# Kernel optimization log

Measured on AMD Instinct MI355X. Metric: run time of the kernel, lower is better.

Reference implementation:

```python
import jax, jax.numpy as jnp
import numpy as np


def _warp_nn(img, flow):
    """Nearest-neighbor warp of one sample.
    img:  [C, D, H, W] channels to deform
    flow: [3, D, H, W] voxel displacements for dims (D, H, W)
    out(p) = img(round(p + flow(p))), indices clamped to the volume.
    """
    D, H, W = img.shape[1:]
    gd = jnp.arange(D, dtype=flow.dtype)[:, None, None]
    gh = jnp.arange(H, dtype=flow.dtype)[None, :, None]
    gw = jnp.arange(W, dtype=flow.dtype)[None, None, :]
    id_ = jnp.clip(jnp.round(gd + flow[0]), 0, D - 1).astype(jnp.int32)
    ih = jnp.clip(jnp.round(gh + flow[1]), 0, H - 1).astype(jnp.int32)
    iw = jnp.clip(jnp.round(gw + flow[2]), 0, W - 1).astype(jnp.int32)
    return img[:, id_, ih, iw]  # gather, [C, D, H, W]


def reference(x, num_steps):
    # scaling: v = x / 2**num_steps
    B, C = x.shape[0], x.shape[1]
    spatial = x.shape[2:]
    v = x / (2.0 ** num_steps)
    # squaring: v <- v + warp(v, v), applied per 3-channel flow group
    warp = jax.vmap(jax.vmap(_warp_nn))  # over batch, then over groups
    for _ in range(num_steps):
        groups = v.reshape(B, C // 3, 3, *spatial)
        vdef = warp(groups, groups).reshape(v.shape)
        v = v + vdef
    return v


def setup_inputs() -> dict:
    key = jax.random.key(0)
    # displacement field in voxel units; scaled so post-scaling steps still move voxels
    x = jax.random.normal(key, (2, 3, 128, 160, 160), dtype=jnp.float32) * 8.0
    return {"x": x, "num_steps": 6}
```

## Files before the change

### kernel.cpp

```cpp
#include <hip/hip_runtime.h>

#define BB 2
#define DD 128
#define HH 160
#define WW 160
constexpr int S   = DD * HH * WW;
constexpr int PL  = HH * WW;
constexpr int VPB = 512;
constexpr int BPP = PL / VPB;
constexpr int NBLK = BB * DD * BPP;
constexpr int PER_XCD = NBLK / 8;

__device__ __forceinline__ int warp_index(int d, int h, int w,
                                          float f0, float f1, float f2) {
    int id = (int)fminf(fmaxf(rintf((float)d + f0), 0.0f), (float)(DD - 1));
    int ih = (int)fminf(fmaxf(rintf((float)h + f1), 0.0f), (float)(HH - 1));
    int iw = (int)fminf(fmaxf(rintf((float)w + f2), 0.0f), (float)(WW - 1));
    return (id * HH + ih) * WW + iw;
}

template <bool IN_SOA, bool OUT_SOA>
__global__ __launch_bounds__(256) void step_k(const float* __restrict__ vin,
                                              float* __restrict__ vout,
                                              float scale) {
    int bid = blockIdx.x;
    int nb  = (bid >> 3) + (bid & 7) * PER_XCD;
    int b   = nb / (DD * BPP);
    int r   = nb - b * (DD * BPP);
    int d   = r / BPP;
    int ip0 = (r - d * BPP) * VPB + threadIdx.x;
    int ip1 = ip0 + 256;

    int w0 = ip0 % WW, h0 = ip0 / WW;
    int w1 = ip1 % WW, h1 = ip1 / WW;
    int p0 = d * PL + ip0;
    int p1 = d * PL + ip1;

    float a0, a1, a2, c0, c1, c2;
    if constexpr (IN_SOA) {
        int s0 = b * 3 * S + p0, s1 = b * 3 * S + p1;
        a0 = vin[s0] * scale; a1 = vin[s0 + S] * scale; a2 = vin[s0 + 2 * S] * scale;
        c0 = vin[s1] * scale; c1 = vin[s1 + S] * scale; c2 = vin[s1 + 2 * S] * scale;
    } else {
        int i0 = (b * S + p0) * 3, i1 = (b * S + p1) * 3;
        a0 = vin[i0] * scale; a1 = vin[i0 + 1] * scale; a2 = vin[i0 + 2] * scale;
        c0 = vin[i1] * scale; c1 = vin[i1 + 1] * scale; c2 = vin[i1 + 2] * scale;
    }

    int q0 = warp_index(d, h0, w0, a0, a1, a2);
    int q1 = warp_index(d, h1, w1, c0, c1, c2);

    float g0, g1, g2, e0, e1, e2;
    if constexpr (IN_SOA) {
        int s0 = b * 3 * S + q0, s1 = b * 3 * S + q1;
        g0 = vin[s0] * scale; g1 = vin[s0 + S] * scale; g2 = vin[s0 + 2 * S] * scale;
        e0 = vin[s1] * scale; e1 = vin[s1 + S] * scale; e2 = vin[s1 + 2 * S] * scale;
    } else {
        int i0 = (b * S + q0) * 3, i1 = (b * S + q1) * 3;
        g0 = vin[i0] * scale; g1 = vin[i0 + 1] * scale; g2 = vin[i0 + 2] * scale;
        e0 = vin[i1] * scale; e1 = vin[i1 + 1] * scale; e2 = vin[i1 + 2] * scale;
    }

    if constexpr (OUT_SOA) {
        int s0 = b * 3 * S + p0, s1 = b * 3 * S + p1;
        vout[s0] = a0 + g0; vout[s0 + S] = a1 + g1; vout[s0 + 2 * S] = a2 + g2;
        vout[s1] = c0 + e0; vout[s1 + S] = c1 + e1; vout[s1 + 2 * S] = c2 + e2;
    } else {
        int i0 = (b * S + p0) * 3, i1 = (b * S + p1) * 3;
        vout[i0] = a0 + g0; vout[i0 + 1] = a1 + g1; vout[i0 + 2] = a2 + g2;
        vout[i1] = c0 + e0; vout[i1 + 1] = c1 + e1; vout[i1 + 2] = c2 + e2;
    }
}

extern "C" void kernel_launch(void* const* d_in, const int* in_sizes, int n_in,
                              void* d_out, int out_size, void* d_ws, size_t ws_size,
                              hipStream_t stream) {
    const float* x = (const float*)d_in[0];
    float* out = (float*)d_out;
    float* ws  = (float*)d_ws;

    step_k<true,  false><<<NBLK, 256, 0, stream>>>(x,   ws,  1.0f / 64.0f);
    step_k<false, false><<<NBLK, 256, 0, stream>>>(ws,  out, 1.0f);
    step_k<false, false><<<NBLK, 256, 0, stream>>>(out, ws,  1.0f);
    step_k<false, false><<<NBLK, 256, 0, stream>>>(ws,  out, 1.0f);
    step_k<false, false><<<NBLK, 256, 0, stream>>>(out, ws,  1.0f);
    step_k<false, true ><<<NBLK, 256, 0, stream>>>(ws,  out, 1.0f);
}
```

Baseline: 268.4 us.

## Fuse pairs of squaring steps into one kernel via recomputed intermediate gathers

Each kernel now performs two scaling-and-squaring steps. The intermediate field at the warped location is rebuilt on the fly from a second-level gather, so only three launches are needed instead of six, and the intermediate full-volume writes and reads go away. Each thread handles four voxels, and interleaved AoS loads and stores use packed 12-byte structs. In exchange, each output needs three dependent random gathers, and more registers are live per thread.

```diff
diff --git a/kernel.cpp b/kernel.cpp
--- a/kernel.cpp
+++ b/kernel.cpp
@@ -6,69 +6,99 @@
 #define WW 160
 constexpr int S   = DD * HH * WW;
 constexpr int PL  = HH * WW;
-constexpr int VPB = 512;
-constexpr int BPP = PL / VPB;
-constexpr int NBLK = BB * DD * BPP;
-constexpr int PER_XCD = NBLK / 8;
+constexpr int K   = 4;
+constexpr int VPB = 256 * K;
+constexpr int TPP = PL / VPB;
+constexpr int NT  = BB * DD * TPP;
+constexpr int PER_XCD = NT / 8;
 
-__device__ __forceinline__ int warp_index(int d, int h, int w,
-                                          float f0, float f1, float f2) {
-    int id = (int)fminf(fmaxf(rintf((float)d + f0), 0.0f), (float)(DD - 1));
-    int ih = (int)fminf(fmaxf(rintf((float)h + f1), 0.0f), (float)(HH - 1));
-    int iw = (int)fminf(fmaxf(rintf((float)w + f2), 0.0f), (float)(WW - 1));
-    return (id * HH + ih) * WW + iw;
+struct __attribute__((packed, aligned(4))) f3 { float x, y, z; };
+
+__device__ __forceinline__ void clamp_idx(int d, int h, int w,
+                                          float f0, float f1, float f2,
+                                          int& od, int& oh, int& ow, int& lin) {
+    od = (int)fminf(fmaxf(rintf((float)d + f0), 0.0f), (float)(DD - 1));
+    oh = (int)fminf(fmaxf(rintf((float)h + f1), 0.0f), (float)(HH - 1));
+    ow = (int)fminf(fmaxf(rintf((float)w + f2), 0.0f), (float)(WW - 1));
+    lin = (od * HH + oh) * WW + ow;
+}
+
+template <bool SOA>
+__device__ __forceinline__ void load3(const float* __restrict__ v, int b, int idx,
+                                      float scale, float* o) {
+    if constexpr (SOA) {
+        int s = b * 3 * S + idx;
+        o[0] = v[s] * scale; o[1] = v[s + S] * scale; o[2] = v[s + 2 * S] * scale;
+    } else {
+        f3 t = *(const f3*)(v + (b * S + idx) * 3);
+        o[0] = t.x; o[1] = t.y; o[2] = t.z;
+    }
 }
 
 template <bool IN_SOA, bool OUT_SOA>
-__global__ __launch_bounds__(256) void step_k(const float* __restrict__ vin,
-                                              float* __restrict__ vout,
-                                              float scale) {
-    int bid = blockIdx.x;
-    int nb  = (bid >> 3) + (bid & 7) * PER_XCD;
-    int b   = nb / (DD * BPP);
-    int r   = nb - b * (DD * BPP);
-    int d   = r / BPP;
-    int ip0 = (r - d * BPP) * VPB + threadIdx.x;
-    int ip1 = ip0 + 256;
+__global__ __launch_bounds__(256) void fused2_k(const float* __restrict__ vin,
+                                                float* __restrict__ vout,
+                                                float scale) {
+    int t  = blockIdx.x;
+    int nb = (t >> 3) + (t & 7) * PER_XCD;
+    int b  = nb / (DD * TPP);
+    int r  = nb - b * (DD * TPP);
+    int d  = r / TPP;
+    int ip0 = (r - d * TPP) * VPB + threadIdx.x;
 
-    int w0 = ip0 % WW, h0 = ip0 / WW;
-    int w1 = ip1 % WW, h1 = ip1 / WW;
-    int p0 = d * PL + ip0;
-    int p1 = d * PL + ip1;
-
-    float a0, a1, a2, c0, c1, c2;
-    if constexpr (IN_SOA) {
-        int s0 = b * 3 * S + p0, s1 = b * 3 * S + p1;
-        a0 = vin[s0] * scale; a1 = vin[s0 + S] * scale; a2 = vin[s0 + 2 * S] * scale;
-        c0 = vin[s1] * scale; c1 = vin[s1 + S] * scale; c2 = vin[s1 + 2 * S] * scale;
-    } else {
-        int i0 = (b * S + p0) * 3, i1 = (b * S + p1) * 3;
-        a0 = vin[i0] * scale; a1 = vin[i0 + 1] * scale; a2 = vin[i0 + 2] * scale;
-        c0 = vin[i1] * scale; c1 = vin[i1 + 1] * scale; c2 = vin[i1 + 2] * scale;
+    int   p[K], h[K], w[K];
+    float a[K][3];
+#pragma unroll
+    for (int k = 0; k < K; ++k) {
+        int ip = ip0 + k * 256;
+        w[k] = ip % WW; h[k] = ip / WW;
+        p[k] = d * PL + ip;
+        load3<IN_SOA>(vin, b, p[k], scale, a[k]);
     }
-
-    int q0 = warp_index(d, h0, w0, a0, a1, a2);
-    int q1 = warp_index(d, h1, w1, c0, c1, c2);
-
-    float g0, g1, g2, e0, e1, e2;
-    if constexpr (IN_SOA) {
-        int s0 = b * 3 * S + q0, s1 = b * 3 * S + q1;
-        g0 = vin[s0] * scale; g1 = vin[s0 + S] * scale; g2 = vin[s0 + 2 * S] * scale;
-        e0 = vin[s1] * scale; e1 = vin[s1 + S] * scale; e2 = vin[s1 + 2 * S] * scale;
-    } else {
-        int i0 = (b * S + q0) * 3, i1 = (b * S + q1) * 3;
-        g0 = vin[i0] * scale; g1 = vin[i0 + 1] * scale; g2 = vin[i0 + 2] * scale;
-        e0 = vin[i1] * scale; e1 = vin[i1 + 1] * scale; e2 = vin[i1 + 2] * scale;
+    int r0i[K];
+#pragma unroll
+    for (int k = 0; k < K; ++k) {
+        int rd, rh, rw;
+        clamp_idx(d, h[k], w[k], a[k][0], a[k][1], a[k][2], rd, rh, rw, r0i[k]);
     }
-
-    if constexpr (OUT_SOA) {
-        int s0 = b * 3 * S + p0, s1 = b * 3 * S + p1;
-        vout[s0] = a0 + g0; vout[s0 + S] = a1 + g1; vout[s0 + 2 * S] = a2 + g2;
-        vout[s1] = c0 + e0; vout[s1 + S] = c1 + e1; vout[s1 + 2 * S] = c2 + e2;
-    } else {
-        int i0 = (b * S + p0) * 3, i1 = (b * S + p1) * 3;
-        vout[i0] = a0 + g0; vout[i0 + 1] = a1 + g1; vout[i0 + 2] = a2 + g2;
-        vout[i1] = c0 + e0; vout[i1 + 1] = c1 + e1; vout[i1 + 2] = c2 + e2;
+    float g[K][3];
+#pragma unroll
+    for (int k = 0; k < K; ++k) load3<IN_SOA>(vin, b, r0i[k], scale, g[k]);
+    float v1[K][3];
+    int r1d[K], r1h[K], r1w[K], r1i[K];
+#pragma unroll
+    for (int k = 0; k < K; ++k) {
+        v1[k][0] = a[k][0] + g[k][0];
+        v1[k][1] = a[k][1] + g[k][1];
+        v1[k][2] = a[k][2] + g[k][2];
+        clamp_idx(d, h[k], w[k], v1[k][0], v1[k][1], v1[k][2],
+                  r1d[k], r1h[k], r1w[k], r1i[k]);
+    }
+    float bb[K][3];
+#pragma unroll
+    for (int k = 0; k < K; ++k) load3<IN_SOA>(vin, b, r1i[k], scale, bb[k]);
+    int r2i[K];
+#pragma unroll
+    for (int k = 0; k < K; ++k) {
+        int rd, rh, rw;
+        clamp_idx(r1d[k], r1h[k], r1w[k], bb[k][0], bb[k][1], bb[k][2],
+                  rd, rh, rw, r2i[k]);
+    }
+    float h2[K][3];
+#pragma unroll
+    for (int k = 0; k < K; ++k) load3<IN_SOA>(vin, b, r2i[k], scale, h2[k]);
+#pragma unroll
+    for (int k = 0; k < K; ++k) {
+        float o0 = v1[k][0] + (bb[k][0] + h2[k][0]);
+        float o1 = v1[k][1] + (bb[k][1] + h2[k][1]);
+        float o2 = v1[k][2] + (bb[k][2] + h2[k][2]);
+        if constexpr (OUT_SOA) {
+            int s = b * 3 * S + p[k];
+            vout[s] = o0; vout[s + S] = o1; vout[s + 2 * S] = o2;
+        } else {
+            f3 v{o0, o1, o2};
+            *(f3*)(vout + (b * S + p[k]) * 3) = v;
+        }
     }
 }
 
@@ -79,10 +109,7 @@
     float* out = (float*)d_out;
     float* ws  = (float*)d_ws;
 
-    step_k<true,  false><<<NBLK, 256, 0, stream>>>(x,   ws,  1.0f / 64.0f);
-    step_k<false, false><<<NBLK, 256, 0, stream>>>(ws,  out, 1.0f);
-    step_k<false, false><<<NBLK, 256, 0, stream>>>(out, ws,  1.0f);
-    step_k<false, false><<<NBLK, 256, 0, stream>>>(ws,  out, 1.0f);
-    step_k<false, false><<<NBLK, 256, 0, stream>>>(out, ws,  1.0f);
-    step_k<false, true ><<<NBLK, 256, 0, stream>>>(ws,  out, 1.0f);
+    fused2_k<true,  false><<<NT, 256, 0, stream>>>(x,   out, 1.0f / 64.0f);
+    fused2_k<false, false><<<NT, 256, 0, stream>>>(out, ws,  1.0f);
+    fused2_k<false, true ><<<NT, 256, 0, stream>>>(ws,  out, 1.0f);
 }
```

New measurement: 273.8 us. 1.02x slower.
